# Optimization experiments

Hardware: AMD Instinct MI355X
Metric: run time of the kernel (lower is better)

## Reference

```python
import jax, jax.numpy as jnp
import numpy as np

def setup_inputs() -> dict:
    key = jax.random.key(0)
    ks = jax.random.split(key, 8)
    B, C, H, W = 4, 64, 64, 64
    Cr = C // 8
    s = 1.0 / np.sqrt(C)
    return {
        "x": jax.random.normal(ks[0], (B, C, H, W), jnp.float32),
        "wq": jax.random.normal(ks[1], (Cr, C), jnp.float32) * s,
        "bq": jax.random.normal(ks[2], (Cr,), jnp.float32) * 0.01,
        "wk": jax.random.normal(ks[3], (Cr, C), jnp.float32) * s,
        "bk": jax.random.normal(ks[4], (Cr,), jnp.float32) * 0.01,
        "wv": jax.random.normal(ks[5], (C, C), jnp.float32) * s,
        "bv": jax.random.normal(ks[6], (C,), jnp.float32) * 0.01,
        "gamma": jax.random.normal(ks[7], (1,), jnp.float32) * 0.1,
    }

def reference(x, wq, bq, wk, bk, wv, bv, gamma):
    B, C, H, W = x.shape
    N = H * W
    xf = x.reshape(B, C, N)  # 1x1 conv == pointwise linear over channel dim
    q = jnp.einsum("oc,bcn->bno", wq, xf) + bq[None, None, :]   # (B, N, Cr)
    k = jnp.einsum("oc,bcn->bon", wk, xf) + bk[None, :, None]   # (B, Cr, N)
    v = jnp.einsum("oc,bcn->bon", wv, xf) + bv[None, :, None]   # (B, C, N)
    attn = jnp.einsum("bno,bom->bnm", q, k)                     # (B, N, N)
    attn = jax.nn.softmax(attn, axis=-1)
    out = jnp.einsum("bcm,bnm->bcn", v, attn)                   # (B, C, N)
    out = out.reshape(B, C, H, W)
    return x + gamma[0] * out
```

## Files before the change

### kernel.cpp

```cpp
#include <hip/hip_runtime.h>

#define BB 4
#define CC 64
#define NN 4096
#define LOG2E 1.44269504088896340736f

typedef __attribute__((ext_vector_type(8)))  short short8;
typedef __attribute__((ext_vector_type(4)))  short short4v;
typedef __attribute__((ext_vector_type(4)))  float f32x4;
typedef __attribute__((ext_vector_type(16))) float f32x16;
typedef unsigned short u16;

#define QWS_ELEMS (BB * NN * 8)

__device__ inline u16 f2bf(float x) {
    unsigned u = __float_as_uint(x);
    u = (u + 0x7fffu + ((u >> 16) & 1u)) >> 16;
    return (u16)u;
}
__device__ inline unsigned pack2rne(float a, float b) {
    return (unsigned)f2bf(a) | ((unsigned)f2bf(b) << 16);
}
__device__ inline unsigned permpack(float lo, float hi) {
    return __builtin_amdgcn_perm(__float_as_uint(hi), __float_as_uint(lo), 0x07060302);
}

union SH8 {
    short8 s;
    struct Halves { short4v lo, hi; } h;
    uint4 u;
};

__global__ __launch_bounds__(512) void proj_kernel(
    const float* __restrict__ x,
    const float* __restrict__ wq, const float* __restrict__ bq,
    const float* __restrict__ wk, const float* __restrict__ bk,
    const float* __restrict__ wv, const float* __restrict__ bv,
    u16* __restrict__ ws_u)
{
    u16* qws = ws_u;
    u16* kws = ws_u + QWS_ELEMS;
    u16* vws = ws_u + 2 * QWS_ELEMS;

    const int y   = blockIdx.y;
    const int pix = blockIdx.x * 512 + threadIdx.x;
    const int b   = pix >> 12;
    const int n   = pix & (NN - 1);
    const float* xb = x + ((size_t)b << 18) + n;

    if (y < 8) {
        const int v0 = y << 3;
        float av[8];
#pragma unroll
        for (int i = 0; i < 8; ++i) av[i] = bv[v0 + i];
#pragma unroll 8
        for (int c = 0; c < CC; ++c) {
            const float xv = xb[(size_t)c << 12];
#pragma unroll
            for (int i = 0; i < 8; ++i)
                av[i] += wv[(v0 + i) * CC + c] * xv;
        }
        u16* vdst = vws + (size_t)b * 262144 + ((n >> 2) << 8) + (n & 3);
#pragma unroll
        for (int i = 0; i < 8; ++i)
            vdst[(v0 + i) << 2] = f2bf(av[i]);
    } else {
        float aq[8], ak[8];
#pragma unroll
        for (int i = 0; i < 8; ++i) { aq[i] = bq[i]; ak[i] = bk[i]; }
#pragma unroll 8
        for (int c = 0; c < CC; ++c) {
            const float xv = xb[(size_t)c << 12];
#pragma unroll
            for (int i = 0; i < 8; ++i) {
                aq[i] += wq[i * CC + c] * xv;
                ak[i] += wk[i * CC + c] * xv;
            }
        }
        uint4 qp, kp;
        qp.x = pack2rne(aq[0] * LOG2E, aq[1] * LOG2E);
        qp.y = pack2rne(aq[2] * LOG2E, aq[3] * LOG2E);
        qp.z = pack2rne(aq[4] * LOG2E, aq[5] * LOG2E);
        qp.w = pack2rne(aq[6] * LOG2E, aq[7] * LOG2E);
        kp.x = pack2rne(ak[0], ak[1]); kp.y = pack2rne(ak[2], ak[3]);
        kp.z = pack2rne(ak[4], ak[5]); kp.w = pack2rne(ak[6], ak[7]);
        *(uint4*)&qws[(size_t)pix * 8] = qp;
        *(uint4*)&kws[(size_t)pix * 8] = kp;
    }
}

__global__ __launch_bounds__(256, 2) void attn_kernel(
    const float* __restrict__ x, const float* __restrict__ gamma,
    const u16* __restrict__ ws_u, float* __restrict__ out)
{
    const u16* qws = ws_u;
    const u16* kws = ws_u + QWS_ELEMS;
    const u16* vws = ws_u + 2 * QWS_ELEMS;

    __shared__ float eb[4 * 1088];
    __shared__ float l_part[4 * 32];
    __shared__ float l_inv[32];

    const int tid  = threadIdx.x;
    const int w    = tid >> 6;
    const int lane = tid & 63;
    const int l31  = lane & 31;
    const int lh   = lane >> 5;

    const int b  = blockIdx.y;
    const int qb = blockIdx.x << 5;
    const int bN = b << 12;

    short8 qf = {0,0,0,0,0,0,0,0};
    if (lane < 32)
        qf = *(const short8*)(qws + (size_t)(bN + qb + l31) * 8);

    const u16* kp = kws + (size_t)(bN + (w << 10) + l31) * 8;
    short8 kf = {0,0,0,0,0,0,0,0}, kn = kf;
    if (lane < 32) kf = *(const short8*)kp;
    kp += 32 * 8;

    const u16* vp = vws + (size_t)b * 262144 + (w << 16);
    const int o00 = (lh << 8) + (l31 << 2);

    SH8 C00, C01, C10, C11, N00, N01, N10, N11;
    C00.h.lo = *(const short4v*)(vp + o00);
    C00.h.hi = *(const short4v*)(vp + o00 + 512);
    C01.h.lo = *(const short4v*)(vp + o00 + 128);
    C01.h.hi = *(const short4v*)(vp + o00 + 640);
    C10.h.lo = *(const short4v*)(vp + o00 + 1024);
    C10.h.hi = *(const short4v*)(vp + o00 + 1536);
    C11.h.lo = *(const short4v*)(vp + o00 + 1152);
    C11.h.hi = *(const short4v*)(vp + o00 + 1664);
    vp += 2048;

    f32x16 z16, acc0, acc1;
#pragma unroll
    for (int r = 0; r < 16; ++r) { z16[r] = 0.f; acc0[r] = 0.f; acc1[r] = 0.f; }
    float ls = 0.f;

    for (int it = 0; it < 32; ++it) {
        N00.h.lo = *(const short4v*)(vp + o00);
        N00.h.hi = *(const short4v*)(vp + o00 + 512);
        N01.h.lo = *(const short4v*)(vp + o00 + 128);
        N01.h.hi = *(const short4v*)(vp + o00 + 640);
        N10.h.lo = *(const short4v*)(vp + o00 + 1024);
        N10.h.hi = *(const short4v*)(vp + o00 + 1536);
        N11.h.lo = *(const short4v*)(vp + o00 + 1152);
        N11.h.hi = *(const short4v*)(vp + o00 + 1664);
        vp += 2048;
        if (lane < 32) kn = *(const short8*)kp;
        kp += 32 * 8;

        f32x16 d = __builtin_amdgcn_mfma_f32_32x32x16_bf16(kf, qf, z16, 0, 0, 0);

        float p[16];
#pragma unroll
        for (int r = 0; r < 16; ++r) p[r] = exp2f(d[r]);
        float s0 = 0.f, s1 = 0.f;
#pragma unroll
        for (int r = 0; r < 8; ++r) { s0 += p[2 * r]; s1 += p[2 * r + 1]; }
        ls += s0 + s1;

        SH8 A0, A1;
        A0.u.x = permpack(p[0],  p[1]);  A0.u.y = permpack(p[2],  p[3]);
        A0.u.z = permpack(p[4],  p[5]);  A0.u.w = permpack(p[6],  p[7]);
        A1.u.x = permpack(p[8],  p[9]);  A1.u.y = permpack(p[10], p[11]);
        A1.u.z = permpack(p[12], p[13]); A1.u.w = permpack(p[14], p[15]);

        acc0 = __builtin_amdgcn_mfma_f32_32x32x16_bf16(A0.s, C00.s, acc0, 0, 0, 0);
        acc1 = __builtin_amdgcn_mfma_f32_32x32x16_bf16(A0.s, C01.s, acc1, 0, 0, 0);
        acc0 = __builtin_amdgcn_mfma_f32_32x32x16_bf16(A1.s, C10.s, acc0, 0, 0, 0);
        acc1 = __builtin_amdgcn_mfma_f32_32x32x16_bf16(A1.s, C11.s, acc1, 0, 0, 0);

        C00 = N00; C01 = N01; C10 = N10; C11 = N11;
        kf = kn;
    }

    float lt = ls + __shfl_xor(ls, 32, 64);
    if (lane < 32) l_part[(w << 5) + l31] = lt;
    __syncthreads();
    if (w == 0 && lane < 32)
        l_inv[l31] = 1.0f / (l_part[l31] + l_part[32 + l31] +
                             l_part[64 + l31] + l_part[96 + l31]);

    if (w >= 2) {
        float* e0 = &eb[(((w - 2) << 1) + 0) * 1088 + lane * 17];
        float* e1 = &eb[(((w - 2) << 1) + 1) * 1088 + lane * 17];
#pragma unroll
        for (int r = 0; r < 16; ++r) { e0[r] = acc0[r]; e1[r] = acc1[r]; }
    }
    __syncthreads();
    if (w < 2) {
        const float* e0 = &eb[((w << 1) + 0) * 1088 + lane * 17];
        const float* e1 = &eb[((w << 1) + 1) * 1088 + lane * 17];
#pragma unroll
        for (int r = 0; r < 16; ++r) { acc0[r] += e0[r]; acc1[r] += e1[r]; }
    }
    __syncthreads();
    if (w == 1) {
        float* e0 = &eb[0 * 1088 + lane * 17];
        float* e1 = &eb[1 * 1088 + lane * 17];
#pragma unroll
        for (int r = 0; r < 16; ++r) { e0[r] = acc0[r]; e1[r] = acc1[r]; }
    }
    __syncthreads();
    if (w == 0) {
        const float* e0 = &eb[0 * 1088 + lane * 17];
        const float* e1 = &eb[1 * 1088 + lane * 17];
#pragma unroll
        for (int r = 0; r < 16; ++r) { acc0[r] += e0[r]; acc1[r] += e1[r]; }

        f32x4 li[4];
#pragma unroll
        for (int k = 0; k < 4; ++k)
            li[k] = *(const f32x4*)&l_inv[(k << 3) + (lh << 2)];
        const float g = gamma[0];
#pragma unroll
        for (int ch = 0; ch < 2; ++ch) {
            const int c = (ch << 5) + l31;
            const f32x16 a = ch ? acc1 : acc0;
            const size_t rowb = (((size_t)((b << 6) + c)) << 12) + qb;
#pragma unroll
            for (int k = 0; k < 4; ++k) {
                const int q0 = (k << 3) + (lh << 2);
                const float4 xv = *(const float4*)&x[rowb + q0];
                float4 o;
                o.x = xv.x + g * a[4 * k + 0] * li[k][0];
                o.y = xv.y + g * a[4 * k + 1] * li[k][1];
                o.z = xv.z + g * a[4 * k + 2] * li[k][2];
                o.w = xv.w + g * a[4 * k + 3] * li[k][3];
                *(float4*)&out[rowb + q0] = o;
            }
        }
    }
}

extern "C" void kernel_launch(void* const* d_in, const int* in_sizes, int n_in,
                              void* d_out, int out_size, void* d_ws, size_t ws_size,
                              hipStream_t stream)
{
    const float* x     = (const float*)d_in[0];
    const float* wq    = (const float*)d_in[1];
    const float* bq    = (const float*)d_in[2];
    const float* wk    = (const float*)d_in[3];
    const float* bk    = (const float*)d_in[4];
    const float* wv    = (const float*)d_in[5];
    const float* bv    = (const float*)d_in[6];
    const float* gamma = (const float*)d_in[7];
    u16*   ws  = (u16*)d_ws;
    float* out = (float*)d_out;

    hipLaunchKernelGGL(proj_kernel, dim3(BB * NN / 512, 9), dim3(512), 0, stream,
                       x, wq, bq, wk, bk, wv, bv, ws);
    hipLaunchKernelGGL(attn_kernel, dim3(NN / 32, BB), dim3(256), 0, stream,
                       x, gamma, ws, out);
}
```

Baseline: 107.8 us.

## Rebalance projection work split, interleave attention blocks across batches, double-buffer fragments

The projection kernel now runs 64-thread blocks over 4 y-slices. One slice computes Q, K and the first 4 V channels, and each of the other three computes 20 V channels, so x is re-read fewer times. The attention kernel uses a 1D grid whose block index is remapped to interleave batches and query chunks, which changes how concurrently resident blocks share K/V in cache. The K/V prefetch now uses indexed ping-pong register arrays with the loop unrolled by 2 instead of copying next-stage registers. The main risks are higher register pressure in proj (20 accumulators) and a less favourable L2 access order.

```diff
diff --git a/kernel.cpp b/kernel.cpp
--- a/kernel.cpp
+++ b/kernel.cpp
@@ -31,7 +31,7 @@
     uint4 u;
 };
 
-__global__ __launch_bounds__(512) void proj_kernel(
+__global__ __launch_bounds__(64) void proj_kernel(
     const float* __restrict__ x,
     const float* __restrict__ wq, const float* __restrict__ bq,
     const float* __restrict__ wk, const float* __restrict__ bk,
@@ -43,31 +43,18 @@
     u16* vws = ws_u + 2 * QWS_ELEMS;
 
     const int y   = blockIdx.y;
-    const int pix = blockIdx.x * 512 + threadIdx.x;
+    const int pix = blockIdx.x * 64 + threadIdx.x;
     const int b   = pix >> 12;
     const int n   = pix & (NN - 1);
     const float* xb = x + ((size_t)b << 18) + n;
-
-    if (y < 8) {
-        const int v0 = y << 3;
-        float av[8];
-#pragma unroll
-        for (int i = 0; i < 8; ++i) av[i] = bv[v0 + i];
-#pragma unroll 8
-        for (int c = 0; c < CC; ++c) {
-            const float xv = xb[(size_t)c << 12];
-#pragma unroll
-            for (int i = 0; i < 8; ++i)
-                av[i] += wv[(v0 + i) * CC + c] * xv;
-        }
-        u16* vdst = vws + (size_t)b * 262144 + ((n >> 2) << 8) + (n & 3);
-#pragma unroll
-        for (int i = 0; i < 8; ++i)
-            vdst[(v0 + i) << 2] = f2bf(av[i]);
-    } else {
-        float aq[8], ak[8];
+    u16* vdst = vws + (size_t)b * 262144 + ((n >> 2) << 8) + (n & 3);
+
+    if (y == 0) {
+        float aq[8], ak[8], av[4];
 #pragma unroll
         for (int i = 0; i < 8; ++i) { aq[i] = bq[i]; ak[i] = bk[i]; }
+#pragma unroll
+        for (int i = 0; i < 4; ++i) av[i] = bv[i];
 #pragma unroll 8
         for (int c = 0; c < CC; ++c) {
             const float xv = xb[(size_t)c << 12];
@@ -76,6 +63,9 @@
                 aq[i] += wq[i * CC + c] * xv;
                 ak[i] += wk[i * CC + c] * xv;
             }
+#pragma unroll
+            for (int i = 0; i < 4; ++i)
+                av[i] += wv[i * CC + c] * xv;
         }
         uint4 qp, kp;
         qp.x = pack2rne(aq[0] * LOG2E, aq[1] * LOG2E);
@@ -86,6 +76,24 @@
         kp.z = pack2rne(ak[4], ak[5]); kp.w = pack2rne(ak[6], ak[7]);
         *(uint4*)&qws[(size_t)pix * 8] = qp;
         *(uint4*)&kws[(size_t)pix * 8] = kp;
+#pragma unroll
+        for (int i = 0; i < 4; ++i)
+            vdst[i << 2] = f2bf(av[i]);
+    } else {
+        const int v0 = y * 20 - 16;
+        float av[20];
+#pragma unroll
+        for (int i = 0; i < 20; ++i) av[i] = bv[v0 + i];
+#pragma unroll 8
+        for (int c = 0; c < CC; ++c) {
+            const float xv = xb[(size_t)c << 12];
+#pragma unroll
+            for (int i = 0; i < 20; ++i)
+                av[i] += wv[(v0 + i) * CC + c] * xv;
+        }
+#pragma unroll
+        for (int i = 0; i < 20; ++i)
+            vdst[(v0 + i) << 2] = f2bf(av[i]);
     }
 }
 
@@ -107,8 +115,10 @@
     const int l31  = lane & 31;
     const int lh   = lane >> 5;
 
-    const int b  = blockIdx.y;
-    const int qb = blockIdx.x << 5;
+    const int i  = blockIdx.x;
+    const int b  = (i >> 1) & 3;
+    const int qc = ((i >> 3) << 1) | (i & 1);
+    const int qb = qc << 5;
     const int bN = b << 12;
 
     short8 qf = {0,0,0,0,0,0,0,0};
@@ -116,43 +126,44 @@
         qf = *(const short8*)(qws + (size_t)(bN + qb + l31) * 8);
 
     const u16* kp = kws + (size_t)(bN + (w << 10) + l31) * 8;
-    short8 kf = {0,0,0,0,0,0,0,0}, kn = kf;
-    if (lane < 32) kf = *(const short8*)kp;
-    kp += 32 * 8;
-
-    const u16* vp = vws + (size_t)b * 262144 + (w << 16);
-    const int o00 = (lh << 8) + (l31 << 2);
-
-    SH8 C00, C01, C10, C11, N00, N01, N10, N11;
-    C00.h.lo = *(const short4v*)(vp + o00);
-    C00.h.hi = *(const short4v*)(vp + o00 + 512);
-    C01.h.lo = *(const short4v*)(vp + o00 + 128);
-    C01.h.hi = *(const short4v*)(vp + o00 + 640);
-    C10.h.lo = *(const short4v*)(vp + o00 + 1024);
-    C10.h.hi = *(const short4v*)(vp + o00 + 1536);
-    C11.h.lo = *(const short4v*)(vp + o00 + 1152);
-    C11.h.hi = *(const short4v*)(vp + o00 + 1664);
-    vp += 2048;
+
+    const u16* vp  = vws + (size_t)b * 262144 + (w << 16);
+    const int  o00 = (lh << 8) + (l31 << 2);
+
+    SH8 F[2][4];
+    short8 kk[2] = {{0,0,0,0,0,0,0,0}, {0,0,0,0,0,0,0,0}};
+
+    F[0][0].h.lo = *(const short4v*)(vp + o00);
+    F[0][0].h.hi = *(const short4v*)(vp + o00 + 512);
+    F[0][1].h.lo = *(const short4v*)(vp + o00 + 128);
+    F[0][1].h.hi = *(const short4v*)(vp + o00 + 640);
+    F[0][2].h.lo = *(const short4v*)(vp + o00 + 1024);
+    F[0][2].h.hi = *(const short4v*)(vp + o00 + 1536);
+    F[0][3].h.lo = *(const short4v*)(vp + o00 + 1152);
+    F[0][3].h.hi = *(const short4v*)(vp + o00 + 1664);
+    if (lane < 32) kk[0] = *(const short8*)kp;
 
     f32x16 z16, acc0, acc1;
 #pragma unroll
     for (int r = 0; r < 16; ++r) { z16[r] = 0.f; acc0[r] = 0.f; acc1[r] = 0.f; }
     float ls = 0.f;
 
+#pragma unroll 2
     for (int it = 0; it < 32; ++it) {
-        N00.h.lo = *(const short4v*)(vp + o00);
-        N00.h.hi = *(const short4v*)(vp + o00 + 512);
-        N01.h.lo = *(const short4v*)(vp + o00 + 128);
-        N01.h.hi = *(const short4v*)(vp + o00 + 640);
-        N10.h.lo = *(const short4v*)(vp + o00 + 1024);
-        N10.h.hi = *(const short4v*)(vp + o00 + 1536);
-        N11.h.lo = *(const short4v*)(vp + o00 + 1152);
-        N11.h.hi = *(const short4v*)(vp + o00 + 1664);
-        vp += 2048;
-        if (lane < 32) kn = *(const short8*)kp;
-        kp += 32 * 8;
-
-        f32x16 d = __builtin_amdgcn_mfma_f32_32x32x16_bf16(kf, qf, z16, 0, 0, 0);
+        const int cur = it & 1, nb = cur ^ 1;
+
+        const u16* vq = vp + (it + 1) * 2048;
+        F[nb][0].h.lo = *(const short4v*)(vq + o00);
+        F[nb][0].h.hi = *(const short4v*)(vq + o00 + 512);
+        F[nb][1].h.lo = *(const short4v*)(vq + o00 + 128);
+        F[nb][1].h.hi = *(const short4v*)(vq + o00 + 640);
+        F[nb][2].h.lo = *(const short4v*)(vq + o00 + 1024);
+        F[nb][2].h.hi = *(const short4v*)(vq + o00 + 1536);
+        F[nb][3].h.lo = *(const short4v*)(vq + o00 + 1152);
+        F[nb][3].h.hi = *(const short4v*)(vq + o00 + 1664);
+        if (lane < 32) kk[nb] = *(const short8*)(kp + (it + 1) * 256);
+
+        f32x16 d = __builtin_amdgcn_mfma_f32_32x32x16_bf16(kk[cur], qf, z16, 0, 0, 0);
 
         float p[16];
 #pragma unroll
@@ -168,13 +179,10 @@
         A1.u.x = permpack(p[8],  p[9]);  A1.u.y = permpack(p[10], p[11]);
         A1.u.z = permpack(p[12], p[13]); A1.u.w = permpack(p[14], p[15]);
 
-        acc0 = __builtin_amdgcn_mfma_f32_32x32x16_bf16(A0.s, C00.s, acc0, 0, 0, 0);
-        acc1 = __builtin_amdgcn_mfma_f32_32x32x16_bf16(A0.s, C01.s, acc1, 0, 0, 0);
-        acc0 = __builtin_amdgcn_mfma_f32_32x32x16_bf16(A1.s, C10.s, acc0, 0, 0, 0);
-        acc1 = __builtin_amdgcn_mfma_f32_32x32x16_bf16(A1.s, C11.s, acc1, 0, 0, 0);
-
-        C00 = N00; C01 = N01; C10 = N10; C11 = N11;
-        kf = kn;
+        acc0 = __builtin_amdgcn_mfma_f32_32x32x16_bf16(A0.s, F[cur][0].s, acc0, 0, 0, 0);
+        acc1 = __builtin_amdgcn_mfma_f32_32x32x16_bf16(A0.s, F[cur][1].s, acc1, 0, 0, 0);
+        acc0 = __builtin_amdgcn_mfma_f32_32x32x16_bf16(A1.s, F[cur][2].s, acc0, 0, 0, 0);
+        acc1 = __builtin_amdgcn_mfma_f32_32x32x16_bf16(A1.s, F[cur][3].s, acc1, 0, 0, 0);
     }
 
     float lt = ls + __shfl_xor(ls, 32, 64);
@@ -251,8 +259,8 @@
     u16*   ws  = (u16*)d_ws;
     float* out = (float*)d_out;
 
-    hipLaunchKernelGGL(proj_kernel, dim3(BB * NN / 512, 9), dim3(512), 0, stream,
+    hipLaunchKernelGGL(proj_kernel, dim3(BB * NN / 64, 4), dim3(64), 0, stream,
                        x, wq, bq, wk, bk, wv, bv, ws);
-    hipLaunchKernelGGL(attn_kernel, dim3(NN / 32, BB), dim3(256), 0, stream,
+    hipLaunchKernelGGL(attn_kernel, dim3(512), dim3(256), 0, stream,
                        x, gamma, ws, out);
 }
```

Result: slower. 110.6 us (+2.6%).

## Shrink attention query tile to 16 using 16x16x32 MFMA and raise occupancy

Applied to the files above, without the earlier changes.

The attention kernel now processes 16 queries per block instead of 32. It uses 16x16x32 bf16 MFMAs for both the score and PV products, with double-buffered K/V register prefetch and a flat 1D grid of twice as many blocks. Launch bounds rise to 4 blocks per CU, and the shared reduction buffers shrink to match. The aim is more parallelism and occupancy to hide memory latency, at the cost of re-reading the K/V stream twice as often overall.

```diff
diff --git a/kernel.cpp b/kernel.cpp
--- a/kernel.cpp
+++ b/kernel.cpp
@@ -8,7 +8,6 @@
 typedef __attribute__((ext_vector_type(8)))  short short8;
 typedef __attribute__((ext_vector_type(4)))  short short4v;
 typedef __attribute__((ext_vector_type(4)))  float f32x4;
-typedef __attribute__((ext_vector_type(16))) float f32x16;
 typedef unsigned short u16;
 
 #define QWS_ELEMS (BB * NN * 8)
@@ -89,7 +88,7 @@
     }
 }
 
-__global__ __launch_bounds__(256, 2) void attn_kernel(
+__global__ __launch_bounds__(256, 4) void attn_kernel(
     const float* __restrict__ x, const float* __restrict__ gamma,
     const u16* __restrict__ ws_u, float* __restrict__ out)
 {
@@ -97,141 +96,134 @@
     const u16* kws = ws_u + QWS_ELEMS;
     const u16* vws = ws_u + 2 * QWS_ELEMS;
 
-    __shared__ float eb[4 * 1088];
-    __shared__ float l_part[4 * 32];
-    __shared__ float l_inv[32];
+    __shared__ float eb[2 * 1088];
+    __shared__ float l_part[4 * 16];
+    __shared__ float l_inv[16];
 
     const int tid  = threadIdx.x;
     const int w    = tid >> 6;
     const int lane = tid & 63;
-    const int l31  = lane & 31;
-    const int lh   = lane >> 5;
-
-    const int b  = blockIdx.y;
-    const int qb = blockIdx.x << 5;
+    const int l15  = lane & 15;
+    const int quad = lane >> 4;
+
+    const int i  = blockIdx.x;
+    const int b  = i >> 8;
+    const int qb = (i & 255) << 4;
     const int bN = b << 12;
 
     short8 qf = {0,0,0,0,0,0,0,0};
-    if (lane < 32)
-        qf = *(const short8*)(qws + (size_t)(bN + qb + l31) * 8);
-
-    const u16* kp = kws + (size_t)(bN + (w << 10) + l31) * 8;
-    short8 kf = {0,0,0,0,0,0,0,0}, kn = kf;
-    if (lane < 32) kf = *(const short8*)kp;
-    kp += 32 * 8;
+    if (lane < 16)
+        qf = *(const short8*)(qws + (size_t)(bN + qb + l15) * 8);
+
+    const u16* kp = kws + (size_t)(bN + (w << 10) + l15) * 8;
 
     const u16* vp = vws + (size_t)b * 262144 + (w << 16);
-    const int o00 = (lh << 8) + (l31 << 2);
-
-    SH8 C00, C01, C10, C11, N00, N01, N10, N11;
-    C00.h.lo = *(const short4v*)(vp + o00);
-    C00.h.hi = *(const short4v*)(vp + o00 + 512);
-    C01.h.lo = *(const short4v*)(vp + o00 + 128);
-    C01.h.hi = *(const short4v*)(vp + o00 + 640);
-    C10.h.lo = *(const short4v*)(vp + o00 + 1024);
-    C10.h.hi = *(const short4v*)(vp + o00 + 1536);
-    C11.h.lo = *(const short4v*)(vp + o00 + 1152);
-    C11.h.hi = *(const short4v*)(vp + o00 + 1664);
-    vp += 2048;
-
-    f32x16 z16, acc0, acc1;
-#pragma unroll
-    for (int r = 0; r < 16; ++r) { z16[r] = 0.f; acc0[r] = 0.f; acc1[r] = 0.f; }
+    const int  og0 = (quad << 8) + (l15 << 2);
+
+    SH8 F[2][4];
+    short8 kk[2][2] = {{{0,0,0,0,0,0,0,0},{0,0,0,0,0,0,0,0}},
+                       {{0,0,0,0,0,0,0,0},{0,0,0,0,0,0,0,0}}};
+
+#pragma unroll
+    for (int g = 0; g < 4; ++g) {
+        F[0][g].h.lo = *(const short4v*)(vp + og0 + (g << 6));
+        F[0][g].h.hi = *(const short4v*)(vp + og0 + (g << 6) + 1024);
+    }
+    if (lane < 16) {
+        kk[0][0] = *(const short8*)(kp);
+        kk[0][1] = *(const short8*)(kp + 128);
+    }
+
+    f32x4 z4 = {0.f, 0.f, 0.f, 0.f};
+    f32x4 acc[4];
+#pragma unroll
+    for (int g = 0; g < 4; ++g) acc[g] = z4;
     float ls = 0.f;
 
+#pragma unroll 2
     for (int it = 0; it < 32; ++it) {
-        N00.h.lo = *(const short4v*)(vp + o00);
-        N00.h.hi = *(const short4v*)(vp + o00 + 512);
-        N01.h.lo = *(const short4v*)(vp + o00 + 128);
-        N01.h.hi = *(const short4v*)(vp + o00 + 640);
-        N10.h.lo = *(const short4v*)(vp + o00 + 1024);
-        N10.h.hi = *(const short4v*)(vp + o00 + 1536);
-        N11.h.lo = *(const short4v*)(vp + o00 + 1152);
-        N11.h.hi = *(const short4v*)(vp + o00 + 1664);
-        vp += 2048;
-        if (lane < 32) kn = *(const short8*)kp;
-        kp += 32 * 8;
-
-        f32x16 d = __builtin_amdgcn_mfma_f32_32x32x16_bf16(kf, qf, z16, 0, 0, 0);
-
-        float p[16];
-#pragma unroll
-        for (int r = 0; r < 16; ++r) p[r] = exp2f(d[r]);
-        float s0 = 0.f, s1 = 0.f;
-#pragma unroll
-        for (int r = 0; r < 8; ++r) { s0 += p[2 * r]; s1 += p[2 * r + 1]; }
-        ls += s0 + s1;
-
-        SH8 A0, A1;
-        A0.u.x = permpack(p[0],  p[1]);  A0.u.y = permpack(p[2],  p[3]);
-        A0.u.z = permpack(p[4],  p[5]);  A0.u.w = permpack(p[6],  p[7]);
-        A1.u.x = permpack(p[8],  p[9]);  A1.u.y = permpack(p[10], p[11]);
-        A1.u.z = permpack(p[12], p[13]); A1.u.w = permpack(p[14], p[15]);
-
-        acc0 = __builtin_amdgcn_mfma_f32_32x32x16_bf16(A0.s, C00.s, acc0, 0, 0, 0);
-        acc1 = __builtin_amdgcn_mfma_f32_32x32x16_bf16(A0.s, C01.s, acc1, 0, 0, 0);
-        acc0 = __builtin_amdgcn_mfma_f32_32x32x16_bf16(A1.s, C10.s, acc0, 0, 0, 0);
-        acc1 = __builtin_amdgcn_mfma_f32_32x32x16_bf16(A1.s, C11.s, acc1, 0, 0, 0);
-
-        C00 = N00; C01 = N01; C10 = N10; C11 = N11;
-        kf = kn;
-    }
-
-    float lt = ls + __shfl_xor(ls, 32, 64);
-    if (lane < 32) l_part[(w << 5) + l31] = lt;
-    __syncthreads();
-    if (w == 0 && lane < 32)
-        l_inv[l31] = 1.0f / (l_part[l31] + l_part[32 + l31] +
-                             l_part[64 + l31] + l_part[96 + l31]);
+        const int cur = it & 1, nb = cur ^ 1;
+
+        const u16* vq = vp + (it + 1) * 2048;
+#pragma unroll
+        for (int g = 0; g < 4; ++g) {
+            F[nb][g].h.lo = *(const short4v*)(vq + og0 + (g << 6));
+            F[nb][g].h.hi = *(const short4v*)(vq + og0 + (g << 6) + 1024);
+        }
+        if (lane < 16) {
+            kk[nb][0] = *(const short8*)(kp + (it + 1) * 256);
+            kk[nb][1] = *(const short8*)(kp + (it + 1) * 256 + 128);
+        }
+
+        f32x4 d0 = __builtin_amdgcn_mfma_f32_16x16x32_bf16(kk[cur][0], qf, z4, 0, 0, 0);
+        f32x4 d1 = __builtin_amdgcn_mfma_f32_16x16x32_bf16(kk[cur][1], qf, z4, 0, 0, 0);
+
+        float p[8];
+#pragma unroll
+        for (int r = 0; r < 4; ++r) { p[r] = exp2f(d0[r]); p[4 + r] = exp2f(d1[r]); }
+        ls += ((p[0] + p[1]) + (p[2] + p[3])) + ((p[4] + p[5]) + (p[6] + p[7]));
+
+        SH8 A;
+        A.u.x = permpack(p[0], p[1]); A.u.y = permpack(p[2], p[3]);
+        A.u.z = permpack(p[4], p[5]); A.u.w = permpack(p[6], p[7]);
+
+#pragma unroll
+        for (int g = 0; g < 4; ++g)
+            acc[g] = __builtin_amdgcn_mfma_f32_16x16x32_bf16(A.s, F[cur][g].s, acc[g], 0, 0, 0);
+    }
+
+    ls += __shfl_xor(ls, 16, 64);
+    ls += __shfl_xor(ls, 32, 64);
+    if (lane < 16) l_part[(w << 4) + l15] = ls;
+    __syncthreads();
+    if (w == 0 && lane < 16)
+        l_inv[l15] = 1.0f / (l_part[l15] + l_part[16 + l15] +
+                             l_part[32 + l15] + l_part[48 + l15]);
 
     if (w >= 2) {
-        float* e0 = &eb[(((w - 2) << 1) + 0) * 1088 + lane * 17];
-        float* e1 = &eb[(((w - 2) << 1) + 1) * 1088 + lane * 17];
-#pragma unroll
-        for (int r = 0; r < 16; ++r) { e0[r] = acc0[r]; e1[r] = acc1[r]; }
+        float* e = &eb[(w - 2) * 1088 + lane * 17];
+#pragma unroll
+        for (int g = 0; g < 4; ++g)
+#pragma unroll
+            for (int r = 0; r < 4; ++r) e[g * 4 + r] = acc[g][r];
     }
     __syncthreads();
     if (w < 2) {
-        const float* e0 = &eb[((w << 1) + 0) * 1088 + lane * 17];
-        const float* e1 = &eb[((w << 1) + 1) * 1088 + lane * 17];
-#pragma unroll
-        for (int r = 0; r < 16; ++r) { acc0[r] += e0[r]; acc1[r] += e1[r]; }
+        const float* e = &eb[w * 1088 + lane * 17];
+#pragma unroll
+        for (int g = 0; g < 4; ++g)
+#pragma unroll
+            for (int r = 0; r < 4; ++r) acc[g][r] += e[g * 4 + r];
     }
     __syncthreads();
     if (w == 1) {
-        float* e0 = &eb[0 * 1088 + lane * 17];
-        float* e1 = &eb[1 * 1088 + lane * 17];
-#pragma unroll
-        for (int r = 0; r < 16; ++r) { e0[r] = acc0[r]; e1[r] = acc1[r]; }
+        float* e = &eb[lane * 17];
+#pragma unroll
+        for (int g = 0; g < 4; ++g)
+#pragma unroll
+            for (int r = 0; r < 4; ++r) e[g * 4 + r] = acc[g][r];
     }
     __syncthreads();
     if (w == 0) {
-        const float* e0 = &eb[0 * 1088 + lane * 17];
-        const float* e1 = &eb[1 * 1088 + lane * 17];
-#pragma unroll
-        for (int r = 0; r < 16; ++r) { acc0[r] += e0[r]; acc1[r] += e1[r]; }
-
-        f32x4 li[4];
-#pragma unroll
-        for (int k = 0; k < 4; ++k)
-            li[k] = *(const f32x4*)&l_inv[(k << 3) + (lh << 2)];
-        const float g = gamma[0];
-#pragma unroll
-        for (int ch = 0; ch < 2; ++ch) {
-            const int c = (ch << 5) + l31;
-            const f32x16 a = ch ? acc1 : acc0;
-            const size_t rowb = (((size_t)((b << 6) + c)) << 12) + qb;
-#pragma unroll
-            for (int k = 0; k < 4; ++k) {
-                const int q0 = (k << 3) + (lh << 2);
-                const float4 xv = *(const float4*)&x[rowb + q0];
-                float4 o;
-                o.x = xv.x + g * a[4 * k + 0] * li[k][0];
-                o.y = xv.y + g * a[4 * k + 1] * li[k][1];
-                o.z = xv.z + g * a[4 * k + 2] * li[k][2];
-                o.w = xv.w + g * a[4 * k + 3] * li[k][3];
-                *(float4*)&out[rowb + q0] = o;
-            }
+        const float* e = &eb[lane * 17];
+#pragma unroll
+        for (int g = 0; g < 4; ++g)
+#pragma unroll
+            for (int r = 0; r < 4; ++r) acc[g][r] += e[g * 4 + r];
+
+        const f32x4 li = *(const f32x4*)&l_inv[quad << 2];
+        const float g0 = gamma[0];
+#pragma unroll
+        for (int g = 0; g < 4; ++g) {
+            const int c = (g << 4) + l15;
+            const size_t base = (((size_t)((b << 6) + c)) << 12) + qb + (quad << 2);
+            const float4 xv = *(const float4*)&x[base];
+            float4 o;
+            o.x = xv.x + g0 * acc[g][0] * li[0];
+            o.y = xv.y + g0 * acc[g][1] * li[1];
+            o.z = xv.z + g0 * acc[g][2] * li[2];
+            o.w = xv.w + g0 * acc[g][3] * li[3];
+            *(float4*)&out[base] = o;
         }
     }
 }
@@ -253,6 +245,6 @@
 
     hipLaunchKernelGGL(proj_kernel, dim3(BB * NN / 512, 9), dim3(512), 0, stream,
                        x, wq, bq, wk, bk, wv, bv, ws);
-    hipLaunchKernelGGL(attn_kernel, dim3(NN / 32, BB), dim3(256), 0, stream,
+    hipLaunchKernelGGL(attn_kernel, dim3(BB * NN / 16), dim3(256), 0, stream,
                        x, gamma, ws, out);
 }
```

New measurement: 124.6 us. +15.6%, slower.
